# Optimization experiments

Measured on AMD Instinct MI355X. Metric: run time of the kernel, lower is better.

The kernel has to match this reference:

```python
import jax, jax.numpy as jnp
import numpy as np

S, B, D = 2048, 2, 1024
H, KV = 16, 4
HD = D // H          # 64
N_REP = H // KV      # 4
EPS = 1e-5
THETA = 10000.0
SCALE = D ** -0.5    # qk_norm_scale = 0.03125 (use_qk_norm path)


def rms_norm(x, w, eps=EPS):
    return x / jnp.sqrt(jnp.mean(x * x, axis=-1, keepdims=True) + eps) * w


def rotate_half(x):
    x1, x2 = jnp.split(x, 2, axis=-1)
    return jnp.concatenate((-x2, x1), axis=-1)


def rope_tables(seq_len, dim, theta=THETA):
    inv_freq = 1.0 / (theta ** (jnp.arange(0, dim, 2, dtype=jnp.float32) / dim))
    t = jnp.arange(seq_len, dtype=jnp.float32)
    freqs = jnp.outer(t, inv_freq)                 # [S, dim/2]
    emb = jnp.concatenate((freqs, freqs), axis=-1)  # [S, dim]
    return jnp.cos(emb), jnp.sin(emb)


def setup_inputs() -> dict:
    key = jax.random.key(0)
    ks = jax.random.split(key, 16)
    s = lambda fan_in: fan_in ** -0.5
    return {
        "x": jax.random.normal(ks[0], (S, B, D), jnp.float32),
        "norm1_w": jnp.ones((D,), jnp.float32),
        "wq": jax.random.normal(ks[1], (D, H * HD), jnp.float32) * s(D),
        "bq": jnp.zeros((H * HD,), jnp.float32),
        "wk": jax.random.normal(ks[2], (D, KV * HD), jnp.float32) * s(D),
        "bk": jnp.zeros((KV * HD,), jnp.float32),
        "wv": jax.random.normal(ks[3], (D, KV * HD), jnp.float32) * s(D),
        "bv": jnp.zeros((KV * HD,), jnp.float32),
        "qn_w": jnp.ones((HD,), jnp.float32),
        "kn_w": jnp.ones((HD,), jnp.float32),
        "wo": jax.random.normal(ks[4], (D, D), jnp.float32) * s(D),
        "bo": jnp.zeros((D,), jnp.float32),
        "norm2_w": jnp.ones((D,), jnp.float32),
        "w1": jax.random.normal(ks[5], (D, 4 * D), jnp.float32) * s(D),
        "b1": jnp.zeros((4 * D,), jnp.float32),
        "w2": jax.random.normal(ks[6], (4 * D, D), jnp.float32) * s(4 * D),
        "b2": jnp.zeros((D,), jnp.float32),
    }


def reference(x, norm1_w, wq, bq, wk, bk, wv, bv, qn_w, kn_w, wo, bo,
              norm2_w, w1, b1, w2, b2):
    # x: [S, B, D] (seq-first, TE convention)
    residual = x
    h = rms_norm(x, norm1_w)
    q = (h @ wq + bq).reshape(S, B, H, HD).transpose(1, 2, 0, 3)    # [B,H,S,HD]
    k = (h @ wk + bk).reshape(S, B, KV, HD).transpose(1, 2, 0, 3)   # [B,KV,S,HD]
    v = (h @ wv + bv).reshape(S, B, KV, HD).transpose(1, 2, 0, 3)
    # GQA: repeat_interleave over head dim
    k = jnp.repeat(k, N_REP, axis=1)  # [B,H,S,HD]
    v = jnp.repeat(v, N_REP, axis=1)
    # per-head QK RMSNorm
    q = rms_norm(q, qn_w)
    k = rms_norm(k, kn_w)
    # RoPE
    cos, sin = rope_tables(S, HD)          # [S,HD] each
    cos = cos[None, None]                  # [1,1,S,HD]
    sin = sin[None, None]
    q = q * cos + rotate_half(q) * sin
    k = k * cos + rotate_half(k) * sin
    # attention with explicit causal mask
    scores = jnp.einsum('bhsd,bhtd->bhst', q, k) * SCALE
    causal = jnp.triu(jnp.ones((S, S), bool), k=1)
    scores = jnp.where(causal, -jnp.inf, scores)
    attn = jax.nn.softmax(scores, axis=-1)
    out = jnp.einsum('bhst,bhtd->bhsd', attn, v)       # [B,H,S,HD]
    out = out.transpose(0, 2, 1, 3).reshape(B, S, D)   # [B,S,D]
    out = out.transpose(1, 0, 2)                       # [S,B,D]
    out = out @ wo + bo
    x = residual + out
    # MLP block (RMSNorm + GELU MLP)
    residual = x
    h2 = rms_norm(x, norm2_w)
    h2 = jax.nn.gelu(h2 @ w1 + b1, approximate=False) @ w2 + b2
    return residual + h2
```

## Files before the change

### kernel.cpp

```cpp
#include <hip/hip_runtime.h>
#include <hip/hip_bf16.h>
#include <math.h>

#define S_LEN 2048
#define BATCH 2
#define DMODEL 1024
#define NH 16
#define NKV 4
#define HDIM 64
#define EPS 1e-5f
#define MROWS (S_LEN*BATCH)
#define QSCALE (0.03125f * 1.44269504088896f)

#define AS1 __attribute__((address_space(1)))
#define AS3 __attribute__((address_space(3)))

typedef __attribute__((ext_vector_type(8))) short bf8_t;
typedef __attribute__((ext_vector_type(4))) float f4_t;
typedef _Float16 __attribute__((ext_vector_type(8))) h8_t;
typedef _Float16 __attribute__((ext_vector_type(4))) h4_t;

#define MFMA16(a,b,c) __builtin_amdgcn_mfma_f32_16x16x16f16(a,b,c,0,0,0)

__device__ __forceinline__ float exp2_fast(float x){ return __builtin_exp2f(x); }

__device__ __forceinline__ unsigned short f2bf(float f){
  __hip_bfloat16 b = __float2bfloat16(f);
  return __builtin_bit_cast(unsigned short, b);
}
__device__ __forceinline__ float bf2f(unsigned short u){
  return __builtin_bit_cast(float, (unsigned)u << 16);
}
__device__ __forceinline__ float gelu_f(float x){
  return 0.5f * x * (1.0f + erff(x * 0.7071067811865475f));
}

__global__ __launch_bounds__(256) void prep_k(const float* __restrict__ wq, const float* __restrict__ wk,
                                              const float* __restrict__ wv, const float* __restrict__ wo,
                                              const float* __restrict__ w1, const float* __restrict__ w2,
                                              __hip_bfloat16* __restrict__ wqkv_t, __hip_bfloat16* __restrict__ wo_t,
                                              __hip_bfloat16* __restrict__ w1_t,   __hip_bfloat16* __restrict__ w2_t,
                                              const float* __restrict__ x, const float* __restrict__ n1w,
                                              __hip_bfloat16* __restrict__ h){
  if (blockIdx.x < 10752){
    __shared__ float t[32][33];
    int b = blockIdx.x;
    const float* src; __hip_bfloat16* dst; int N, stride, nx;
    if (b < 1024)      { src=wq; dst=wqkv_t;               N=1024; stride=1024; nx=32;  }
    else if (b < 1280) { b-=1024; src=wk; dst=wqkv_t+1024*1024; N=256; stride=1024; nx=8; }
    else if (b < 1536) { b-=1280; src=wv; dst=wqkv_t+1280*1024; N=256; stride=1024; nx=8; }
    else if (b < 2560) { b-=1536; src=wo; dst=wo_t;        N=1024; stride=1024; nx=32;  }
    else if (b < 6656) { b-=2560; src=w1; dst=w1_t;        N=4096; stride=1024; nx=128; }
    else               { b-=6656; src=w2; dst=w2_t;        N=1024; stride=4096; nx=32;  }
    int n0 = (b % nx)*32, k0 = (b / nx)*32;
    int tx = threadIdx.x & 31, ty = threadIdx.x >> 5;
    #pragma unroll
    for (int i = 0; i < 4; ++i)
      t[ty*4+i][tx] = src[(size_t)(k0+ty*4+i)*N + n0 + tx];
    __syncthreads();
    #pragma unroll
    for (int i = 0; i < 4; ++i)
      dst[(size_t)(n0+ty*4+i)*stride + k0 + tx] = __float2bfloat16(t[tx][ty*4+i]);
  } else {
    __shared__ float sm[5];
    size_t row = blockIdx.x - 10752;
    const float4* xr = (const float4*)(x + row * DMODEL);
    float4 v = xr[threadIdx.x];
    float ss = v.x*v.x + v.y*v.y + v.z*v.z + v.w*v.w;
    #pragma unroll
    for (int off = 32; off; off >>= 1) ss += __shfl_down(ss, off);
    if ((threadIdx.x & 63) == 0) sm[threadIdx.x >> 6] = ss;
    __syncthreads();
    if (threadIdx.x == 0) sm[4] = rsqrtf((sm[0]+sm[1]+sm[2]+sm[3]) * (1.0f/DMODEL) + EPS);
    __syncthreads();
    float r = sm[4];
    float4 wv4 = ((const float4*)n1w)[threadIdx.x];
    ushort4 ob;
    ob.x = f2bf(v.x*r*wv4.x); ob.y = f2bf(v.y*r*wv4.y);
    ob.z = f2bf(v.z*r*wv4.z); ob.w = f2bf(v.w*r*wv4.w);
    ((ushort4*)(h + row * DMODEL))[threadIdx.x] = ob;
  }
}

template<int EPI, bool DB>
__global__ __launch_bounds__(256) void mgemm_k(const __hip_bfloat16* __restrict__ A,
                                               const __hip_bfloat16* __restrict__ Wt,
                                               const float* __restrict__ bias,
                                               __hip_bfloat16* __restrict__ Cb,
                                               int N, int Kstride, int kLen, int sy){
  __shared__ __align__(16) __hip_bfloat16 As[DB?2:1][8192];
  __shared__ __align__(16) __hip_bfloat16 Bs[DB?2:1][8192];
  const int tid = threadIdx.x;
  const int w = tid >> 6, l = tid & 63;
  const int lr = l & 15, lc = l >> 4;
  const int lr7 = lr & 7;
  const int rrow = l >> 3;
  const int kch  = (l & 7) ^ rrow;

  const unsigned gx = gridDim.x, gy = gridDim.y;
  unsigned hb  = (blockIdx.z * gy + blockIdx.y) * gx + blockIdx.x;
  unsigned xcd = hb & 7u;
  unsigned i   = hb >> 3;
  unsigned cgPerX = (gx * gridDim.z) >> 3;
  unsigned stSz = cgPerX * (unsigned)sy;
  unsigned st  = i / stSz, rr2 = i % stSz;
  unsigned cgl = rr2 % cgPerX, yy = rr2 / cgPerX;
  unsigned byi = st * (unsigned)sy + yy;
  unsigned cg  = xcd * cgPerX + cgl;
  unsigned bxi = cg % gx;
  unsigned bzi = cg / gx;

  const int bm = byi * 128, bn = bxi * 128;
  const int wm = (w >> 1) * 64, wn = (w & 1) * 64;
  const int kOff = bzi * kLen;

  const __hip_bfloat16* Ag = A  + (size_t)(bm + 32*w + rrow)*Kstride + kOff + kch*8;
  const __hip_bfloat16* Bg = Wt + (size_t)(bn + 32*w + rrow)*Kstride + kOff + kch*8;

  f4_t acc[4][4] = {};

  auto stage = [&](int buf, int k0){
    #pragma unroll
    for (int ii = 0; ii < 4; ++ii){
      __builtin_amdgcn_global_load_lds((const AS1 void*)(Ag + (size_t)(8*ii)*Kstride + k0),
                                       (AS3 void*)(&As[buf][w*2048 + ii*512 + l*8]), 16, 0, 0);
      __builtin_amdgcn_global_load_lds((const AS1 void*)(Bg + (size_t)(8*ii)*Kstride + k0),
                                       (AS3 void*)(&Bs[buf][w*2048 + ii*512 + l*8]), 16, 0, 0);
    }
  };

  auto compute = [&](int buf){
    #pragma unroll
    for (int s = 0; s < 2; ++s){
      const int kx = (s*32 + lc*8) ^ (lr7*8);
      bf8_t af[4], bfr[4];
      #pragma unroll
      for (int mi = 0; mi < 4; ++mi)
        af[mi] = *(const bf8_t*)(&As[buf][(wm + mi*16 + lr)*64 + kx]);
      #pragma unroll
      for (int ni = 0; ni < 4; ++ni)
        bfr[ni] = *(const bf8_t*)(&Bs[buf][(wn + ni*16 + lr)*64 + kx]);
      #pragma unroll
      for (int mi = 0; mi < 4; ++mi)
        #pragma unroll
        for (int ni = 0; ni < 4; ++ni)
          acc[mi][ni] = __builtin_amdgcn_mfma_f32_16x16x32_bf16(af[mi], bfr[ni], acc[mi][ni], 0, 0, 0);
    }
  };

  if constexpr (DB){
    const int nt = kLen >> 6;
    stage(0, 0);
    asm volatile("s_waitcnt vmcnt(0)" ::: "memory");
    __builtin_amdgcn_s_barrier();
    int cur = 0;
    for (int t = 0; t < nt; ++t){
      if (t + 1 < nt) stage(cur ^ 1, (t + 1) << 6);
      compute(cur);
      asm volatile("s_waitcnt vmcnt(0)" ::: "memory");
      __builtin_amdgcn_s_barrier();
      cur ^= 1;
    }
  } else {
    for (int k0 = 0; k0 < kLen; k0 += 64){
      __syncthreads();
      stage(0, k0);
      __syncthreads();
      compute(0);
    }
  }

  __hip_bfloat16* Cp = (EPI == 3) ? (Cb + (size_t)bzi * ((size_t)MROWS * N)) : Cb;

  #pragma unroll
  for (int ni = 0; ni < 4; ++ni){
    int col = bn + wn + ni*16 + lr;
    float bb = (EPI == 3) ? 0.0f : bias[col];
    #pragma unroll
    for (int mi = 0; mi < 4; ++mi){
      #pragma unroll
      for (int r = 0; r < 4; ++r){
        int row = bm + wm + mi*16 + lc*4 + r;
        size_t off = (size_t)row * N + col;
        float v = acc[mi][ni][r] + bb;
        if (EPI == 1) Cp[off] = __float2bfloat16(gelu_f(v));
        else          Cp[off] = __float2bfloat16(v);
      }
    }
  }
}

template<int NS>
__global__ __launch_bounds__(256) void reduce_k(const unsigned short* __restrict__ P,
                                                const float* __restrict__ bias,
                                                const float* __restrict__ res,
                                                float* __restrict__ out, int N){
  size_t i = ((size_t)blockIdx.x*256 + threadIdx.x) * 4;
  int col = (int)(i % (size_t)N);
  size_t stride = (size_t)MROWS * N;
  float a0=0,a1=0,a2=0,a3=0;
  #pragma unroll
  for (int p = 0; p < NS; ++p){
    ushort4 u = *(const ushort4*)(P + p*stride + i);
    a0 += bf2f(u.x); a1 += bf2f(u.y); a2 += bf2f(u.z); a3 += bf2f(u.w);
  }
  float4 bb = *(const float4*)(bias + col);
  float4 r4 = *(const float4*)(res + i);
  float4 o = make_float4(a0+bb.x+r4.x, a1+bb.y+r4.y, a2+bb.z+r4.z, a3+bb.w+r4.w);
  *(float4*)(out + i) = o;
}

template<int NS>
__global__ __launch_bounds__(256) void redn_k(const unsigned short* __restrict__ P,
                                              const float* __restrict__ bias,
                                              const float* __restrict__ res,
                                              const float* __restrict__ nw,
                                              float* __restrict__ x1,
                                              __hip_bfloat16* __restrict__ h){
  __shared__ float sm[5];
  size_t row = blockIdx.x;
  size_t i = row * DMODEL + threadIdx.x*4;
  size_t stride = (size_t)MROWS * DMODEL;
  float4 bb = *(const float4*)(bias + threadIdx.x*4);
  float4 r4 = *(const float4*)(res + i);
  float4 v = make_float4(bb.x+r4.x, bb.y+r4.y, bb.z+r4.z, bb.w+r4.w);
  #pragma unroll
  for (int p = 0; p < NS; ++p){
    ushort4 u = *(const ushort4*)(P + p*stride + i);
    v.x += bf2f(u.x); v.y += bf2f(u.y); v.z += bf2f(u.z); v.w += bf2f(u.w);
  }
  *(float4*)(x1 + i) = v;
  float ss = v.x*v.x + v.y*v.y + v.z*v.z + v.w*v.w;
  #pragma unroll
  for (int off = 32; off; off >>= 1) ss += __shfl_down(ss, off);
  if ((threadIdx.x & 63) == 0) sm[threadIdx.x >> 6] = ss;
  __syncthreads();
  if (threadIdx.x == 0) sm[4] = rsqrtf((sm[0]+sm[1]+sm[2]+sm[3]) * (1.0f/DMODEL) + EPS);
  __syncthreads();
  float r = sm[4];
  float4 wv = ((const float4*)nw)[threadIdx.x];
  ushort4 ob;
  ob.x = f2bf(v.x*r*wv.x); ob.y = f2bf(v.y*r*wv.y);
  ob.z = f2bf(v.z*r*wv.z); ob.w = f2bf(v.w*r*wv.w);
  ((ushort4*)(h + row * DMODEL))[threadIdx.x] = ob;
}

__global__ __launch_bounds__(64) void rope2_k(const unsigned short* __restrict__ P,
                                              const float* __restrict__ bq, const float* __restrict__ bk,
                                              const float* __restrict__ qw, const float* __restrict__ kw,
                                              _Float16* __restrict__ qo, _Float16* __restrict__ ko){
  const int s = blockIdx.x;
  const int y = blockIdx.y;
  const int b = y / 20, r0 = y % 20;
  const bool isQ = (r0 < 16);
  const int hh = isQ ? r0 : (r0 - 16);
  const int col0 = isQ ? hh*64 : 1024 + hh*64;
  const int lane = threadIdx.x;
  const size_t pstride = (size_t)MROWS * 1536;
  size_t off = ((size_t)s * BATCH + b) * 1536 + col0 + lane;
  float v = bf2f(P[off]) + bf2f(P[off + pstride])
          + (isQ ? bq[hh*64 + lane] : bk[hh*64 + lane]);
  float ss = v * v;
  #pragma unroll
  for (int m = 32; m; m >>= 1) ss += __shfl_xor(ss, m);
  float rr = rsqrtf(ss * (1.0f/64.0f) + EPS);
  v = v * rr * (isQ ? qw[lane] : kw[lane]);
  int i = lane & 31;
  float invf = powf(10000.0f, -((float)(2*i)) * (1.0f/64.0f));
  float ang = (float)s * invf;
  float c, sn;
  sincosf(ang, &sn, &c);
  float partner = __shfl_xor(v, 32);
  float rh = (lane < 32) ? -partner : partner;
  float o = (v * c + rh * sn) * (isQ ? QSCALE : 1.0f);
  _Float16* outp = isQ ? (qo + (((size_t)b * NH  + hh) * S_LEN + s) * 64 + lane)
                       : (ko + (((size_t)b * NKV + hh) * S_LEN + s) * 64 + lane);
  *outp = (_Float16)o;
}

__global__ __launch_bounds__(256) void vcast_k(const unsigned short* __restrict__ P,
                                               const float* __restrict__ bv,
                                               _Float16* __restrict__ Vt){
  __shared__ float t[64][65];
  const int s0 = blockIdx.x * 64;
  const int bkv = blockIdx.y;
  const int b = bkv >> 2, kv = bkv & 3;
  const int tid = threadIdx.x;
  const size_t pstride = (size_t)MROWS * 1536;
  #pragma unroll
  for (int i = 0; i < 16; ++i){
    int idx = tid + 256*i;
    int sl = idx >> 6, d = idx & 63;
    size_t off = ((size_t)(s0+sl)*BATCH + b)*1536 + 1280 + kv*64 + d;
    t[d][sl] = bf2f(P[off]) + bf2f(P[off + pstride]) + bv[kv*64 + d];
  }
  __syncthreads();
  #pragma unroll
  for (int i = 0; i < 16; ++i){
    int idx = tid + 256*i;
    int d = idx >> 6, sl = idx & 63;
    Vt[((size_t)bkv*64 + d)*S_LEN + s0 + sl] = (_Float16)t[d][sl];
  }
}

__global__ __launch_bounds__(256) void attn2_k(const _Float16* __restrict__ Q,
                                               const _Float16* __restrict__ K,
                                               const _Float16* __restrict__ Vt,
                                               __hip_bfloat16* __restrict__ AO){
  __shared__ __align__(16) _Float16 Ks[8*512];
  __shared__ __align__(16) _Float16 Vs[8*512];
  const int bh = blockIdx.x;
  const int qb = (gridDim.y - 1) - blockIdx.y;
  const int b = bh >> 4, h = bh & 15;
  const int kvh = h >> 2;
  const int tid = threadIdx.x;
  const int w = tid >> 6, l = tid & 63;
  const int lr = l & 15, quad = l >> 4;

  const _Float16* qp = Q + ((size_t)bh * S_LEN + qb*64 + w*16 + lr) * 64;
  h8_t qf0 = *(const h8_t*)(qp + quad*8);
  h8_t qf1 = *(const h8_t*)(qp + 32 + quad*8);

  const _Float16* kbase = K  + (size_t)(b*NKV + kvh) * S_LEN * 64;
  const _Float16* vbase = Vt + (size_t)(b*NKV + kvh) * 64 * S_LEN;

  f4_t Od[4] = {};
  float m_i = -3.0e38f, l_i = 0.0f;

  for (int kt = 0; kt <= qb; ++kt){
    __syncthreads();
    #pragma unroll
    for (int ii = 0; ii < 4; ++ii){
      int i = w*4 + ii;
      if (i < 8){
        int cc = i >> 1, dh = i & 1;
        const _Float16* src = kbase + (size_t)(kt*64 + cc*16 + lr)*64 + dh*32 + quad*8;
        __builtin_amdgcn_global_load_lds((const AS1 void*)src, (AS3 void*)(Ks + i*512), 16, 0, 0);
      } else {
        int j = i - 8;
        int dd = j >> 1, cc32 = j & 1;
        const _Float16* src = vbase + (size_t)(dd*16 + lr)*S_LEN + kt*64 + cc32*32 + quad*8;
        __builtin_amdgcn_global_load_lds((const AS1 void*)src, (AS3 void*)(Vs + j*512), 16, 0, 0);
      }
    }
    __syncthreads();

    const bool diag = (kt == qb);
    f4_t sc[4];
    #pragma unroll
    for (int nc2 = 0; nc2 < 4; ++nc2){
      if (diag && nc2 > w){
        sc[nc2][0] = -1.0e30f; sc[nc2][1] = -1.0e30f;
        sc[nc2][2] = -1.0e30f; sc[nc2][3] = -1.0e30f;
        continue;
      }
      f4_t a = {};
      h8_t k0 = *(const h8_t*)(Ks + (nc2*2+0)*512 + l*8);
      h8_t k1 = *(const h8_t*)(Ks + (nc2*2+1)*512 + l*8);
      a = __builtin_amdgcn_mfma_f32_16x16x32_f16(k0, qf0, a, 0, 0, 0);
      a = __builtin_amdgcn_mfma_f32_16x16x32_f16(k1, qf1, a, 0, 0, 0);
      if (diag && nc2 == w){
        #pragma unroll
        for (int r = 0; r < 4; ++r)
          if (quad*4 + r > lr) a[r] = -1.0e30f;
      }
      sc[nc2] = a;
    }

    float mx = sc[0][0];
    #pragma unroll
    for (int nc2 = 0; nc2 < 4; ++nc2)
      #pragma unroll
      for (int r = 0; r < 4; ++r) mx = fmaxf(mx, sc[nc2][r]);
    mx = fmaxf(mx, __shfl_xor(mx, 16));
    mx = fmaxf(mx, __shfl_xor(mx, 32));
    float nm = fmaxf(mx, m_i);
    float alpha = exp2_fast(m_i - nm);
    m_i = nm;
    float rs = 0.0f;
    h4_t pf[4];
    #pragma unroll
    for (int nc2 = 0; nc2 < 4; ++nc2)
      #pragma unroll
      for (int r = 0; r < 4; ++r){
        float e = exp2_fast(sc[nc2][r] - nm);
        rs += e;
        pf[nc2][r] = (_Float16)e;
      }
    rs += __shfl_xor(rs, 16);
    rs += __shfl_xor(rs, 32);
    l_i = l_i * alpha + rs;
    #pragma unroll
    for (int dd = 0; dd < 4; ++dd)
      #pragma unroll
      for (int r = 0; r < 4; ++r) Od[dd][r] *= alpha;

    #pragma unroll
    for (int dd = 0; dd < 4; ++dd)
      #pragma unroll
      for (int nc2 = 0; nc2 < 4; ++nc2){
        if (diag && nc2 > w) continue;
        h4_t vf = *(const h4_t*)(Vs + (dd*2 + (nc2>>1))*512
                                 + (((nc2&1)*2 + (quad>>1))*16 + lr)*8 + (quad&1)*4);
        Od[dd] = MFMA16(vf, pf[nc2], Od[dd]);
      }
  }

  float inv = 1.0f / l_i;
  #pragma unroll
  for (int dd = 0; dd < 4; ++dd){
    ushort4 w4;
    w4.x = f2bf(Od[dd][0]*inv); w4.y = f2bf(Od[dd][1]*inv);
    w4.z = f2bf(Od[dd][2]*inv); w4.w = f2bf(Od[dd][3]*inv);
    size_t sg = (size_t)qb*64 + w*16 + lr;
    *(ushort4*)(AO + (sg*BATCH + b)*DMODEL + h*64 + dd*16 + quad*4) = w4;
  }
}

extern "C" void kernel_launch(void* const* d_in, const int* in_sizes, int n_in,
                              void* d_out, int out_size, void* d_ws, size_t ws_size,
                              hipStream_t stream){
  const float* x   = (const float*)d_in[0];
  const float* n1w = (const float*)d_in[1];
  const float* wq  = (const float*)d_in[2];
  const float* bq  = (const float*)d_in[3];
  const float* wk  = (const float*)d_in[4];
  const float* bk  = (const float*)d_in[5];
  const float* wv  = (const float*)d_in[6];
  const float* bv  = (const float*)d_in[7];
  const float* qnw = (const float*)d_in[8];
  const float* knw = (const float*)d_in[9];
  const float* wo  = (const float*)d_in[10];
  const float* bo  = (const float*)d_in[11];
  const float* n2w = (const float*)d_in[12];
  const float* w1  = (const float*)d_in[13];
  const float* b1  = (const float*)d_in[14];
  const float* w2  = (const float*)d_in[15];
  const float* b2  = (const float*)d_in[16];
  float* out = (float*)d_out;

  char* p = (char*)d_ws;
  auto carve = [&](size_t bytes)->char*{ char* r = p; p += (bytes + 255) & ~(size_t)255; return r; };
  __hip_bfloat16* h_bf   = (__hip_bfloat16*)carve((size_t)MROWS*DMODEL*2);
  __hip_bfloat16* ao_bf  = (__hip_bfloat16*)carve((size_t)MROWS*DMODEL*2);
  __hip_bfloat16* mid_bf = (__hip_bfloat16*)carve((size_t)MROWS*4096*2);
  __hip_bfloat16* wqkv_t = (__hip_bfloat16*)carve((size_t)1536*1024*2);
  __hip_bfloat16* wo_t   = (__hip_bfloat16*)carve((size_t)1024*1024*2);
  __hip_bfloat16* w1_t   = (__hip_bfloat16*)carve((size_t)4096*1024*2);
  __hip_bfloat16* w2_t   = (__hip_bfloat16*)carve((size_t)1024*4096*2);
  char* scratch = carve((size_t)2*MROWS*1536*2);
  __hip_bfloat16* qkv_p = (__hip_bfloat16*)scratch;
  __hip_bfloat16* ps    = (__hip_bfloat16*)scratch;
  _Float16* q_f  = (_Float16*)carve((size_t)BATCH*NH *S_LEN*64*2);
  _Float16* k_f  = (_Float16*)carve((size_t)BATCH*NKV*S_LEN*64*2);
  _Float16* vt_f = (_Float16*)carve((size_t)BATCH*NKV*64*S_LEN*2);
  float* x1   = (float*)carve((size_t)MROWS*DMODEL*4);

  prep_k<<<10752 + MROWS, 256, 0, stream>>>(wq, wk, wv, wo, w1, w2,
                                            wqkv_t, wo_t, w1_t, w2_t, x, n1w, h_bf);

  mgemm_k<3,true><<<dim3(12, 32, 2), 256, 0, stream>>>(h_bf, wqkv_t, nullptr, qkv_p, 1536, 1024, 512, 8);

  rope2_k<<<dim3(S_LEN, BATCH*20), 64, 0, stream>>>((const unsigned short*)qkv_p, bq, bk, qnw, knw, q_f, k_f);
  vcast_k<<<dim3(S_LEN/64, BATCH*NKV), 256, 0, stream>>>((const unsigned short*)qkv_p, bv, vt_f);
  attn2_k<<<dim3(BATCH*NH, S_LEN/64), 256, 0, stream>>>(q_f, k_f, vt_f, ao_bf);

  mgemm_k<3,true><<<dim3(8, 32, 2), 256, 0, stream>>>(ao_bf, wo_t, nullptr, ps, 1024, 1024, 512, 8);
  redn_k<2><<<MROWS, 256, 0, stream>>>((const unsigned short*)ps, bo, x, n2w, x1, h_bf);

  mgemm_k<1,true><<<dim3(32, 32, 1), 256, 0, stream>>>(h_bf, w1_t, b1, mid_bf, 4096, 1024, 1024, 8);

  mgemm_k<3,false><<<dim3(8, 32, 2), 256, 0, stream>>>(mid_bf, w2_t, nullptr, ps, 1024, 4096, 2048, 4);
  reduce_k<2><<<4096, 256, 0, stream>>>((const unsigned short*)ps, b2, x1, out, 1024);
}
```

Baseline: 369.7 us.

## Drop GEMM double buffering and add lazy softmax rescaling in attention

Removes the double-buffered LDS staging path from the GEMM kernel, so the QKV, output-projection and W1 GEMMs now use the single-buffer loop with two barriers per K tile. In attention, the running max and the accumulator rescale are updated only when some lane's new row max exceeds the stored max by more than 8 (in log2 units), which skips the exp and multiplies on most tiles. The GEMM change halves LDS use, which may raise occupancy, but loses the overlap of loads with MFMA work. The lazy rescale lets unnormalised exponentials reach up to 2^8 in fp16, which fits in fp16 range.

```diff
diff --git a/kernel.cpp b/kernel.cpp
--- a/kernel.cpp
+++ b/kernel.cpp
@@ -82,14 +82,14 @@
   }
 }
 
-template<int EPI, bool DB>
+template<int EPI>
 __global__ __launch_bounds__(256) void mgemm_k(const __hip_bfloat16* __restrict__ A,
                                                const __hip_bfloat16* __restrict__ Wt,
                                                const float* __restrict__ bias,
                                                __hip_bfloat16* __restrict__ Cb,
                                                int N, int Kstride, int kLen, int sy){
-  __shared__ __align__(16) __hip_bfloat16 As[DB?2:1][8192];
-  __shared__ __align__(16) __hip_bfloat16 Bs[DB?2:1][8192];
+  __shared__ __align__(16) __hip_bfloat16 As[8192];
+  __shared__ __align__(16) __hip_bfloat16 Bs[8192];
   const int tid = threadIdx.x;
   const int w = tid >> 6, l = tid & 63;
   const int lr = l & 15, lc = l >> 4;
@@ -119,27 +119,27 @@
 
   f4_t acc[4][4] = {};
 
-  auto stage = [&](int buf, int k0){
+  auto stage = [&](int k0){
     #pragma unroll
     for (int ii = 0; ii < 4; ++ii){
       __builtin_amdgcn_global_load_lds((const AS1 void*)(Ag + (size_t)(8*ii)*Kstride + k0),
-                                       (AS3 void*)(&As[buf][w*2048 + ii*512 + l*8]), 16, 0, 0);
+                                       (AS3 void*)(&As[w*2048 + ii*512 + l*8]), 16, 0, 0);
       __builtin_amdgcn_global_load_lds((const AS1 void*)(Bg + (size_t)(8*ii)*Kstride + k0),
-                                       (AS3 void*)(&Bs[buf][w*2048 + ii*512 + l*8]), 16, 0, 0);
+                                       (AS3 void*)(&Bs[w*2048 + ii*512 + l*8]), 16, 0, 0);
     }
   };
 
-  auto compute = [&](int buf){
+  auto compute = [&](){
     #pragma unroll
     for (int s = 0; s < 2; ++s){
       const int kx = (s*32 + lc*8) ^ (lr7*8);
       bf8_t af[4], bfr[4];
       #pragma unroll
       for (int mi = 0; mi < 4; ++mi)
-        af[mi] = *(const bf8_t*)(&As[buf][(wm + mi*16 + lr)*64 + kx]);
+        af[mi] = *(const bf8_t*)(&As[(wm + mi*16 + lr)*64 + kx]);
       #pragma unroll
       for (int ni = 0; ni < 4; ++ni)
-        bfr[ni] = *(const bf8_t*)(&Bs[buf][(wn + ni*16 + lr)*64 + kx]);
+        bfr[ni] = *(const bf8_t*)(&Bs[(wn + ni*16 + lr)*64 + kx]);
       #pragma unroll
       for (int mi = 0; mi < 4; ++mi)
         #pragma unroll
@@ -148,26 +148,11 @@
     }
   };
 
-  if constexpr (DB){
-    const int nt = kLen >> 6;
-    stage(0, 0);
-    asm volatile("s_waitcnt vmcnt(0)" ::: "memory");
-    __builtin_amdgcn_s_barrier();
-    int cur = 0;
-    for (int t = 0; t < nt; ++t){
-      if (t + 1 < nt) stage(cur ^ 1, (t + 1) << 6);
-      compute(cur);
-      asm volatile("s_waitcnt vmcnt(0)" ::: "memory");
-      __builtin_amdgcn_s_barrier();
-      cur ^= 1;
-    }
-  } else {
-    for (int k0 = 0; k0 < kLen; k0 += 64){
-      __syncthreads();
-      stage(0, k0);
-      __syncthreads();
-      compute(0);
-    }
+  for (int k0 = 0; k0 < kLen; k0 += 64){
+    __syncthreads();
+    stage(k0);
+    __syncthreads();
+    compute();
   }
 
   __hip_bfloat16* Cp = (EPI == 3) ? (Cb + (size_t)bzi * ((size_t)MROWS * N)) : Cb;
@@ -374,26 +359,29 @@
       for (int r = 0; r < 4; ++r) mx = fmaxf(mx, sc[nc2][r]);
     mx = fmaxf(mx, __shfl_xor(mx, 16));
     mx = fmaxf(mx, __shfl_xor(mx, 32));
-    float nm = fmaxf(mx, m_i);
-    float alpha = exp2_fast(m_i - nm);
-    m_i = nm;
+    if (!__all(mx <= m_i + 8.0f)){
+      float nm = fmaxf(mx, m_i);
+      float alpha = exp2_fast(m_i - nm);
+      m_i = nm;
+      l_i *= alpha;
+      #pragma unroll
+      for (int dd = 0; dd < 4; ++dd)
+        #pragma unroll
+        for (int r = 0; r < 4; ++r) Od[dd][r] *= alpha;
+    }
     float rs = 0.0f;
     h4_t pf[4];
     #pragma unroll
     for (int nc2 = 0; nc2 < 4; ++nc2)
       #pragma unroll
       for (int r = 0; r < 4; ++r){
-        float e = exp2_fast(sc[nc2][r] - nm);
+        float e = exp2_fast(sc[nc2][r] - m_i);
         rs += e;
         pf[nc2][r] = (_Float16)e;
       }
     rs += __shfl_xor(rs, 16);
     rs += __shfl_xor(rs, 32);
-    l_i = l_i * alpha + rs;
-    #pragma unroll
-    for (int dd = 0; dd < 4; ++dd)
-      #pragma unroll
-      for (int r = 0; r < 4; ++r) Od[dd][r] *= alpha;
+    l_i += rs;
 
     #pragma unroll
     for (int dd = 0; dd < 4; ++dd)
@@ -459,17 +447,17 @@
   prep_k<<<10752 + MROWS, 256, 0, stream>>>(wq, wk, wv, wo, w1, w2,
                                             wqkv_t, wo_t, w1_t, w2_t, x, n1w, h_bf);
 
-  mgemm_k<3,true><<<dim3(12, 32, 2), 256, 0, stream>>>(h_bf, wqkv_t, nullptr, qkv_p, 1536, 1024, 512, 8);
+  mgemm_k<3><<<dim3(12, 32, 2), 256, 0, stream>>>(h_bf, wqkv_t, nullptr, qkv_p, 1536, 1024, 512, 8);
 
   rope2_k<<<dim3(S_LEN, BATCH*20), 64, 0, stream>>>((const unsigned short*)qkv_p, bq, bk, qnw, knw, q_f, k_f);
   vcast_k<<<dim3(S_LEN/64, BATCH*NKV), 256, 0, stream>>>((const unsigned short*)qkv_p, bv, vt_f);
   attn2_k<<<dim3(BATCH*NH, S_LEN/64), 256, 0, stream>>>(q_f, k_f, vt_f, ao_bf);
 
-  mgemm_k<3,true><<<dim3(8, 32, 2), 256, 0, stream>>>(ao_bf, wo_t, nullptr, ps, 1024, 1024, 512, 8);
+  mgemm_k<3><<<dim3(8, 32, 2), 256, 0, stream>>>(ao_bf, wo_t, nullptr, ps, 1024, 1024, 512, 8);
   redn_k<2><<<MROWS, 256, 0, stream>>>((const unsigned short*)ps, bo, x, n2w, x1, h_bf);
 
-  mgemm_k<1,true><<<dim3(32, 32, 1), 256, 0, stream>>>(h_bf, w1_t, b1, mid_bf, 4096, 1024, 1024, 8);
-
-  mgemm_k<3,false><<<dim3(8, 32, 2), 256, 0, stream>>>(mid_bf, w2_t, nullptr, ps, 1024, 4096, 2048, 4);
+  mgemm_k<1><<<dim3(32, 32, 1), 256, 0, stream>>>(h_bf, w1_t, b1, mid_bf, 4096, 1024, 1024, 8);
+
+  mgemm_k<3><<<dim3(8, 32, 2), 256, 0, stream>>>(mid_bf, w2_t, nullptr, ps, 1024, 4096, 2048, 4);
   reduce_k<2><<<4096, 256, 0, stream>>>((const unsigned short*)ps, b2, x1, out, 1024);
 }
```

Measured after the change: 384.6 us. 1.04x slower.
